# Optimization experiments

Hardware: AMD Instinct MI355X
Metric: run time of the kernel (lower is better)

Reference implementation:

```python
import jax, jax.numpy as jnp
import numpy as np

D_MODEL = 1024
N_HEADS = 16
HEAD_DIM = D_MODEL // N_HEADS
ROPE_BASE = 10000.0


def setup_inputs() -> dict:
    key = jax.random.key(0)
    k1, k2, k3 = jax.random.split(key, 3)
    B, T = 4, 2048
    s = 0.02
    x = jax.random.normal(k1, (B, T, D_MODEL), dtype=jnp.float32)
    w_qkv = jax.random.normal(k2, (D_MODEL, 3 * D_MODEL), dtype=jnp.float32) * s
    b_qkv = jnp.zeros((3 * D_MODEL,), dtype=jnp.float32)
    w_out = jax.random.normal(k3, (D_MODEL, D_MODEL), dtype=jnp.float32) * s
    b_out = jnp.zeros((D_MODEL,), dtype=jnp.float32)
    return {"x": x, "w_qkv": w_qkv, "b_qkv": b_qkv, "w_out": w_out, "b_out": b_out}


def _rope(q, k):
    # q, k: [B, H, T, D]; standard rotate-half RoPE, base 10000
    T, D = q.shape[-2], q.shape[-1]
    inv_freq = 1.0 / (ROPE_BASE ** (jnp.arange(0, D, 2, dtype=jnp.float32) / D))
    freqs = jnp.arange(T, dtype=jnp.float32)[:, None] * inv_freq[None, :]  # [T, D/2]
    emb = jnp.concatenate([freqs, freqs], axis=-1)                         # [T, D]
    cos, sin = jnp.cos(emb), jnp.sin(emb)

    def rot_half(x):
        x1, x2 = x[..., : D // 2], x[..., D // 2 :]
        return jnp.concatenate([-x2, x1], axis=-1)

    q = q * cos + rot_half(q) * sin
    k = k * cos + rot_half(k) * sin
    return q, k


def reference(x, w_qkv, b_qkv, w_out, b_out):
    B, T, C = x.shape
    H, D = N_HEADS, HEAD_DIM
    qkv = x @ w_qkv + b_qkv                      # [B, T, 3C]
    q, k, v = jnp.split(qkv, 3, axis=-1)
    # [B, T, C] -> [B, H, T, D]
    q = q.reshape(B, T, H, D).transpose(0, 2, 1, 3)
    k = k.reshape(B, T, H, D).transpose(0, 2, 1, 3)
    v = v.reshape(B, T, H, D).transpose(0, 2, 1, 3)
    q, k = _rope(q, k)
    scores = jnp.einsum("bhqd,bhkd->bhqk", q, k) / jnp.sqrt(jnp.asarray(D, x.dtype))
    causal = jnp.tril(jnp.ones((T, T), dtype=bool))
    scores = jnp.where(causal, scores, jnp.asarray(-1e30, scores.dtype))
    attn = jax.nn.softmax(scores, axis=-1)
    out = jnp.einsum("bhqk,bhkd->bhqd", attn, v)  # [B, H, T, D]
    out = out.transpose(0, 2, 1, 3).reshape(B, T, C)
    return out @ w_out + b_out
```

## Files before the change

kernel.cpp:

```cpp
#include <hip/hip_runtime.h>
#include <stdint.h>

#define B_SZ 4
#define T_SZ 2048
#define H_SZ 16
#define D_SZ 64
#define C_SZ 1024
#define N3_SZ 3072
#define M_SZ (B_SZ * T_SZ)

using bf16x8 = __attribute__((ext_vector_type(8))) __bf16;
using f32x4  = __attribute__((ext_vector_type(4))) float;
using f32x16 = __attribute__((ext_vector_type(16))) float;
using uivec2 = __attribute__((ext_vector_type(2))) unsigned int;
using uivec4 = __attribute__((ext_vector_type(4))) unsigned int;

__device__ __forceinline__ unsigned short f2bf(float f) {
    union { float f; unsigned int u; } v; v.f = f;
    unsigned int r = v.u + 0x7FFFu + ((v.u >> 16) & 1u);
    return (unsigned short)(r >> 16);
}
__device__ __forceinline__ unsigned int pack_bf2(float lo, float hi) {
    return (unsigned int)f2bf(lo) | ((unsigned int)f2bf(hi) << 16);
}

__device__ __forceinline__ void async16(const void* g, void* l) {
    __builtin_amdgcn_global_load_lds((const __attribute__((address_space(1))) void*)g,
                                     (__attribute__((address_space(3))) void*)l, 16, 0, 0);
}
__device__ __forceinline__ f32x4 mfma16(bf16x8 a, bf16x8 b, f32x4 c) {
    return __builtin_amdgcn_mfma_f32_16x16x32_bf16(a, b, c, 0, 0, 0);
}
__device__ __forceinline__ f32x16 mfma32(bf16x8 a, bf16x8 b, f32x16 c) {
    return __builtin_amdgcn_mfma_f32_32x32x16_bf16(a, b, c, 0, 0, 0);
}
__device__ __forceinline__ f32x16 zero16() {
    f32x16 z;
#pragma unroll
    for (int i = 0; i < 16; i++) z[i] = 0.f;
    return z;
}

__global__ void k_f32_to_bf16(const float4* __restrict__ in, uint2* __restrict__ out, int n4) {
    int i = blockIdx.x * blockDim.x + threadIdx.x;
    int stride = gridDim.x * blockDim.x;
    for (; i < n4; i += stride) {
        float4 v = in[i];
        uint2 o;
        o.x = pack_bf2(v.x, v.y);
        o.y = pack_bf2(v.z, v.w);
        out[i] = o;
    }
}

__global__ void k_transpose_bf16(const float* __restrict__ in, unsigned short* __restrict__ out,
                                 int K, int N) {
    __shared__ float tile[32][33];
    int n0 = blockIdx.x * 32, k0 = blockIdx.y * 32;
    int tx = threadIdx.x & 31, ty = threadIdx.x >> 5;
#pragma unroll
    for (int j = 0; j < 32; j += 8)
        tile[ty + j][tx] = in[(size_t)(k0 + ty + j) * N + (n0 + tx)];
    __syncthreads();
#pragma unroll
    for (int j = 0; j < 32; j += 8)
        out[(size_t)(n0 + ty + j) * K + (k0 + tx)] = f2bf(tile[tx][ty + j]);
}

__global__ void k_transpose_v(const unsigned short* __restrict__ qkv,
                              unsigned short* __restrict__ vt) {
    __shared__ unsigned short tile[32][36];
    int t0 = blockIdx.x * 32, d0 = blockIdx.y * 32, bh = blockIdx.z;
    int b = bh >> 4, h = bh & 15;
    int row = threadIdx.x >> 3, ch = threadIdx.x & 7;
    const unsigned short* src =
        qkv + (size_t)(b * T_SZ + t0 + row) * N3_SZ + 2 * C_SZ + h * D_SZ + d0 + ch * 4;
    *(uint2*)&tile[row][ch * 4] = *(const uint2*)src;
    __syncthreads();
    unsigned short o[4];
#pragma unroll
    for (int i = 0; i < 4; i++) o[i] = tile[ch * 4 + i][row];
    *(uint2*)(vt + ((size_t)bh * 64 + d0 + row) * T_SZ + t0 + ch * 4) = *(uint2*)o;
}

__global__ void k_rope_table(float* __restrict__ rtab) {
    int i = blockIdx.x * blockDim.x + threadIdx.x;
    if (i >= T_SZ * 32) return;
    int t = i >> 5, fq = i & 31;
    float invf = powf(10000.0f, -(float)fq / 32.0f);
    float ang = (float)t * invf;
    rtab[t * 64 + fq * 2]     = cosf(ang);
    rtab[t * 64 + fq * 2 + 1] = sinf(ang);
}

#define GEMM_PHASE_TAIL()                                    \
    __builtin_amdgcn_s_barrier();                            \
    asm volatile("s_waitcnt lgkmcnt(0)" ::: "memory");       \
    __builtin_amdgcn_sched_barrier(0);                       \
    __builtin_amdgcn_s_setprio(1);

#define GEMM_PHASE_END()                                     \
    __builtin_amdgcn_s_setprio(0);                           \
    __builtin_amdgcn_s_barrier();

#define MFMA8(MF, A0, A1)                                    \
    acc[MF][0] = mfma16(A0, b00, acc[MF][0]);                \
    acc[MF][1] = mfma16(A0, b10, acc[MF][1]);                \
    acc[MF][2] = mfma16(A0, b20, acc[MF][2]);                \
    acc[MF][3] = mfma16(A0, b30, acc[MF][3]);                \
    acc[MF][0] = mfma16(A1, b01, acc[MF][0]);                \
    acc[MF][1] = mfma16(A1, b11, acc[MF][1]);                \
    acc[MF][2] = mfma16(A1, b21, acc[MF][2]);                \
    acc[MF][3] = mfma16(A1, b31, acc[MF][3]);

#define GEMM_BODY(Kdim)                                                                    \
    const int tid = threadIdx.x;                                                           \
    const int wave = tid >> 6, lane = tid & 63;                                            \
    const int lcol = lane & 15, lrow = lane >> 4;                                          \
    const int wm = wave >> 2, wn = wave & 3;                                               \
    const int sx = lcol & 7;                                                               \
    const int srow = tid >> 3;                                                             \
    const int sch = (tid & 7) ^ (srow & 7);                                                \
    const unsigned short* Asrc = A + (size_t)(m0 + srow) * (Kdim) + sch * 8;               \
    const unsigned short* Bsrc = BT + (size_t)(n0 + srow) * (Kdim) + sch * 8;              \
    const int ldst = tid * 8;                                                              \
    f32x4 acc[4][4];                                                                       \
    _Pragma("unroll") for (int i = 0; i < 4; i++)                                          \
        _Pragma("unroll") for (int j = 0; j < 4; j++) acc[i][j] = (f32x4){0.f,0.f,0.f,0.f};\
    SU_B(0,0,0); SU_B(0,1,0); SU_B(0,2,0); SU_B(0,3,0); SU_A(0,0,0); SU_A(0,1,0);          \
    SU_B(1,0,64); SU_B(1,1,64); SU_B(1,2,64); SU_B(1,3,64); SU_A(1,0,64); SU_A(1,1,64);    \
    asm volatile("s_waitcnt vmcnt(6)" ::: "memory");                                       \
    __builtin_amdgcn_s_barrier();                                                          \
    const int NT = (Kdim) >> 6;                                                            \
    for (int t = 0; t < NT; ++t) {                                                         \
        const int cur = t % 3;                                                             \
        int nx2 = cur + 2; if (nx2 >= 3) nx2 -= 3;                                         \
        const unsigned short* Acur = As + cur * 8192;                                      \
        const unsigned short* Bcur = Bs + cur * 16384;                                     \
        const size_t kn = (size_t)(t + 2) * 64;                                            \
        const bool more2 = (t + 2 < NT);                                                   \
        bf16x8 b00, b01, b10, b11, b20, b21, b30, b31;                                     \
        {                                                                                  \
            bf16x8 a0 = LD_A(0, 0), a1 = LD_A(0, 1);                                       \
            b00 = LD_B(0, 0); b01 = LD_B(0, 1);                                            \
            b10 = LD_B(1, 0); b11 = LD_B(1, 1);                                            \
            b20 = LD_B(2, 0); b21 = LD_B(2, 1);                                            \
            b30 = LD_B(3, 0); b31 = LD_B(3, 1);                                            \
            if (more2) { SU_B(nx2, 0, kn); SU_B(nx2, 1, kn); }                             \
            GEMM_PHASE_TAIL(); MFMA8(0, a0, a1); GEMM_PHASE_END();                         \
        }                                                                                  \
        {                                                                                  \
            bf16x8 a0 = LD_A(1, 0), a1 = LD_A(1, 1);                                       \
            if (more2) { SU_B(nx2, 2, kn); SU_B(nx2, 3, kn); }                             \
            GEMM_PHASE_TAIL(); MFMA8(1, a0, a1); GEMM_PHASE_END();                         \
        }                                                                                  \
        {                                                                                  \
            bf16x8 a0 = LD_A(2, 0), a1 = LD_A(2, 1);                                       \
            if (more2) { SU_A(nx2, 0, kn); }                                               \
            GEMM_PHASE_TAIL(); MFMA8(2, a0, a1); GEMM_PHASE_END();                         \
        }                                                                                  \
        {                                                                                  \
            bf16x8 a0 = LD_A(3, 0), a1 = LD_A(3, 1);                                       \
            if (more2) { SU_A(nx2, 1, kn); }                                               \
            if (more2) asm volatile("s_waitcnt vmcnt(6)" ::: "memory");                    \
            else       asm volatile("s_waitcnt vmcnt(0)" ::: "memory");                    \
            GEMM_PHASE_TAIL(); MFMA8(3, a0, a1); GEMM_PHASE_END();                         \
        }                                                                                  \
    }

#define SU_A(BI, Q, KO) async16(Asrc + (size_t)(Q) * 64 * KD + (KO), \
                                As + (BI) * 8192 + (Q) * 4096 + ldst)
#define SU_B(BI, Q, KO) async16(Bsrc + (size_t)(Q) * 64 * KD + (KO), \
                                Bs + (BI) * 16384 + (Q) * 4096 + ldst)
#define LD_A(MF, KS) (*reinterpret_cast<const bf16x8*>( \
    Acur + ((wm * 64 + (MF) * 16 + lcol)) * 64 + ((((KS) * 4 + lrow) ^ sx) * 8)))
#define LD_B(NF, KS) (*reinterpret_cast<const bf16x8*>( \
    Bcur + ((wn * 64 + (NF) * 16 + lcol)) * 64 + ((((KS) * 4 + lrow) ^ sx) * 8)))

__global__ __launch_bounds__(512, 2) void k_gemmqkv(const unsigned short* __restrict__ A,
                                                    const unsigned short* __restrict__ BT,
                                                    const float* __restrict__ bias,
                                                    unsigned short* __restrict__ qkv,
                                                    const float* __restrict__ rtab) {
    extern __shared__ unsigned short lds[];
    unsigned short* As = lds;
    unsigned short* Bs = lds + 3 * 8192;
#define KD C_SZ
    int orig = blockIdx.x + gridDim.x * blockIdx.y;
    int lin = (orig & 7) * 96 + (orig >> 3);
    const int n0 = (lin % 12) * 256, m0 = (lin / 12) * 128;
    GEMM_BODY(C_SZ)
#undef KD

    const int cb = n0 + wn * 64;
    float bv[4];
#pragma unroll
    for (int nf = 0; nf < 4; nf++) bv[nf] = bias[cb + nf * 16 + lcol];
    if (cb < 2 * C_SZ) {
        const float scl = (cb < C_SZ) ? 0.125f * 1.4426950408889634f : 1.0f;
#pragma unroll
        for (int mf = 0; mf < 4; mf++) {
#pragma unroll
            for (int r = 0; r < 4; r++) {
                int row = m0 + wm * 64 + mf * 16 + lrow * 4 + r;
                int t = row & (T_SZ - 1);
#pragma unroll
                for (int p = 0; p < 2; p++) {
                    int fq = p * 16 + lcol;
                    float2 cs = *(const float2*)(rtab + t * 64 + fq * 2);
                    float a  = acc[mf][p][r]     + bv[p];
                    float bb = acc[mf][p + 2][r] + bv[p + 2];
                    float lo = (a * cs.x - bb * cs.y) * scl;
                    float hi = (bb * cs.x + a * cs.y) * scl;
                    qkv[(size_t)row * N3_SZ + cb + fq]      = f2bf(lo);
                    qkv[(size_t)row * N3_SZ + cb + fq + 32] = f2bf(hi);
                }
            }
        }
    } else {
#pragma unroll
        for (int nf = 0; nf < 4; nf++) {
#pragma unroll
            for (int mf = 0; mf < 4; mf++) {
#pragma unroll
                for (int r = 0; r < 4; r++) {
                    int row = m0 + wm * 64 + mf * 16 + lrow * 4 + r;
                    qkv[(size_t)row * N3_SZ + cb + nf * 16 + lcol] =
                        f2bf(acc[mf][nf][r] + bv[nf]);
                }
            }
        }
    }
}

__global__ __launch_bounds__(512, 2) void k_gemmout(const unsigned short* __restrict__ A,
                                                    const unsigned short* __restrict__ BT,
                                                    const float* __restrict__ bias,
                                                    float* __restrict__ Cout) {
    extern __shared__ unsigned short lds[];
    unsigned short* As = lds;
    unsigned short* Bs = lds + 3 * 8192;
#define KD C_SZ
    int orig = blockIdx.x + gridDim.x * blockIdx.y;
    int lin = (orig & 7) * 32 + (orig >> 3);
    const int n0 = (lin % 4) * 256, m0 = (lin / 4) * 128;
    GEMM_BODY(C_SZ)
#undef KD
    const int cb = n0 + wn * 64;
#pragma unroll
    for (int nf = 0; nf < 4; nf++) {
        int col = cb + nf * 16 + lcol;
        float bv = bias[col];
#pragma unroll
        for (int mf = 0; mf < 4; mf++) {
#pragma unroll
            for (int r = 0; r < 4; r++) {
                int row = m0 + wm * 64 + mf * 16 + lrow * 4 + r;
                Cout[(size_t)row * C_SZ + col] = acc[mf][nf][r] + bv;
            }
        }
    }
}

#undef SU_A
#undef SU_B
#undef LD_A
#undef LD_B

__global__ __launch_bounds__(512, 4) void k_attn(const unsigned short* __restrict__ qkv,
                                                 const unsigned short* __restrict__ vt,
                                                 unsigned short* __restrict__ attn_out) {
    __shared__ __align__(16) unsigned short lds[16384];
    int orig = blockIdx.x + gridDim.x * blockIdx.y;
    int lin = (orig & 7) * 64 + (orig >> 3);
    const int pr = lin & 7, bh = lin >> 3;
    const int b = bh >> 4, h = bh & 15;
    const int qtA = pr, qtB = 15 - pr;
    const int tid = threadIdx.x;
    const int w = tid >> 6, lane = tid & 63;
    const int l31 = lane & 31, hi = lane >> 5;
    const int sx = l31 & 7;
    const int wsel = w >> 2;
    const int wq0 = (wsel ? qtB : qtA) * 128 + (w & 3) * 32;
    const int qg = wq0 + l31;

    const size_t gbase = (size_t)b * T_SZ * N3_SZ;
    const size_t vbase = (size_t)bh * 64 * T_SZ;

#pragma unroll
    for (int L = 0; L < 4; L++) {
        int flat = L * 512 + tid;
        int row = flat >> 3, ch = flat & 7;
        int qrow = (row < 128) ? (qtA * 128 + row) : (qtB * 128 + row - 128);
        int chs = ch ^ (row & 7);
        async16(qkv + gbase + (size_t)qrow * N3_SZ + h * D_SZ + chs * 8, lds + flat * 8);
    }
    asm volatile("s_waitcnt vmcnt(0)" ::: "memory");
    __builtin_amdgcn_s_barrier();
    bf16x8 qf[4];
#pragma unroll
    for (int s = 0; s < 4; s++)
        qf[s] = *reinterpret_cast<const bf16x8*>(
            lds + wsel * 8192 + ((w & 3) * 32 + l31) * 64 + ((2 * s + hi) ^ sx) * 8);
    asm volatile("s_waitcnt lgkmcnt(0)" ::: "memory");
    __builtin_amdgcn_sched_barrier(0);
    __builtin_amdgcn_s_barrier();

    const int srow = tid >> 3;
    const int schs = (tid & 7) ^ (srow & 7);
    const unsigned short* ksrc0 = qkv + gbase + (size_t)srow * N3_SZ + C_SZ + h * D_SZ + schs * 8;
    const unsigned short* vsrc0 = vt + vbase + (size_t)srow * T_SZ + schs * 8;
#define STAGE(KV0, BI)                                                      \
    do {                                                                    \
        async16(ksrc0 + (size_t)(KV0) * N3_SZ, lds + (BI) * 8192 + tid * 8);\
        async16(vsrc0 + (KV0), lds + (BI) * 8192 + 4096 + tid * 8);         \
    } while (0)

    f32x16 accO[2];
    accO[0] = zero16();
    accO[1] = zero16();
    float lsum = 0.f;

    STAGE(0, 0);
    const int nkv = 32 - 2 * pr;
    for (int kv = 0; kv < nkv; kv++) {
        const int cur = kv & 1;
        const int kv0 = kv * 64;
        if (kv + 1 < nkv) {
            STAGE(kv0 + 64, cur ^ 1);
            asm volatile("s_waitcnt vmcnt(2)" ::: "memory");
        } else {
            asm volatile("s_waitcnt vmcnt(0)" ::: "memory");
        }
        __builtin_amdgcn_s_barrier();
        asm volatile("" ::: "memory");

        if (kv0 <= wq0 + 31) {
            const unsigned short* Kb = lds + cur * 8192;
            const unsigned short* Vb = lds + cur * 8192 + 4096;
            const bool diag = (kv0 + 63) > wq0;
            __builtin_amdgcn_s_setprio(1);
#pragma unroll
            for (int kk = 0; kk < 2; kk++) {
                f32x16 sc = zero16();
                const unsigned short* krow = Kb + (kk * 32 + l31) * 64;
#pragma unroll
                for (int s = 0; s < 4; s++) {
                    bf16x8 kf = *reinterpret_cast<const bf16x8*>(krow + ((2 * s + hi) ^ sx) * 8);
                    sc = mfma32(kf, qf[s], sc);
                }
                const int kvkk = kv0 + kk * 32 + 4 * hi;
                unsigned int wd[4][2];
#pragma unroll
                for (int i = 0; i < 16; i += 2) {
                    float p0 = __builtin_amdgcn_exp2f(sc[i]);
                    float p1 = __builtin_amdgcn_exp2f(sc[i + 1]);
                    if (diag) {
                        int kg = kvkk + (i & 3) + 8 * (i >> 2);
                        p0 = (kg > qg) ? 0.f : p0;
                        p1 = (kg + 1 > qg) ? 0.f : p1;
                    }
                    lsum += p0 + p1;
                    unsigned int wv;
                    asm("v_cvt_pk_bf16_f32 %0, %1, %2" : "=v"(wv) : "v"(p0), "v"(p1));
                    wd[i >> 2][(i >> 1) & 1] = wv;
                }
#pragma unroll
                for (int s = 0; s < 2; s++) {
                    uivec2 r0 = __builtin_amdgcn_permlane32_swap(wd[2 * s][0], wd[2 * s + 1][0],
                                                                 false, false);
                    uivec2 r1 = __builtin_amdgcn_permlane32_swap(wd[2 * s][1], wd[2 * s + 1][1],
                                                                 false, false);
                    uivec4 frv = {r0.x, r1.x, r0.y, r1.y};
                    bf16x8 pfrag = __builtin_bit_cast(bf16x8, frv);
                    const int ks = kk * 2 + s;
#pragma unroll
                    for (int dt = 0; dt < 2; dt++) {
                        bf16x8 vf = *reinterpret_cast<const bf16x8*>(
                            Vb + (dt * 32 + l31) * 64 + ((2 * ks + hi) ^ sx) * 8);
                        accO[dt] = mfma32(vf, pfrag, accO[dt]);
                    }
                }
            }
            __builtin_amdgcn_s_setprio(0);
        }
        asm volatile("" ::: "memory");
        __builtin_amdgcn_s_barrier();
    }
#undef STAGE

    __syncthreads();
    float lt = lsum + __shfl_xor(lsum, 32, 64);
    float linv = 1.0f / lt;
    unsigned int* ow = (unsigned int*)lds + w * 1024;
#pragma unroll
    for (int dt = 0; dt < 2; dt++) {
#pragma unroll
        for (int i = 0; i < 16; i += 2) {
            float v0 = accO[dt][i] * linv;
            float v1 = accO[dt][i + 1] * linv;
            unsigned int wv;
            asm("v_cvt_pk_bf16_f32 %0, %1, %2" : "=v"(wv) : "v"(v0), "v"(v1));
            int idx = ((i & 3) + 8 * (i >> 2) + 4 * hi + 32 * dt) >> 1;
            ow[l31 * 32 + (idx ^ (sx << 2))] = wv;
        }
    }
    int q2 = lane >> 1;
    int c0 = (lane & 1) * 4;
    unsigned short* orow = attn_out + (size_t)(b * T_SZ + wq0 + q2) * C_SZ + h * D_SZ;
#pragma unroll
    for (int j = 0; j < 4; j++) {
        int c = c0 + j;
        uint4 val = *(const uint4*)(ow + q2 * 32 + ((c ^ (q2 & 7)) * 4));
        *(uint4*)(orow + c * 8) = val;
    }
}

extern "C" void kernel_launch(void* const* d_in, const int* in_sizes, int n_in,
                              void* d_out, int out_size, void* d_ws, size_t ws_size,
                              hipStream_t stream) {
    (void)in_sizes; (void)n_in; (void)out_size;
    const float* x     = (const float*)d_in[0];
    const float* w_qkv = (const float*)d_in[1];
    const float* b_qkv = (const float*)d_in[2];
    const float* w_out = (const float*)d_in[3];
    const float* b_out = (const float*)d_in[4];
    float* out = (float*)d_out;

    unsigned short* xb    = (unsigned short*)d_ws;
    unsigned short* wqkvT = xb + (size_t)M_SZ * C_SZ;
    unsigned short* woutT = wqkvT + (size_t)N3_SZ * C_SZ;
    unsigned short* qkv   = woutT + (size_t)C_SZ * C_SZ;
    unsigned short* attn  = qkv + (size_t)M_SZ * N3_SZ;
    float* rtab = (float*)(attn + (size_t)M_SZ * C_SZ);
    unsigned short* vtb = xb;
    size_t needed = (size_t)((char*)(rtab + T_SZ * 64) - (char*)d_ws);
    if (ws_size < needed) return;

    hipFuncSetAttribute((const void*)k_gemmqkv,
                        hipFuncAttributeMaxDynamicSharedMemorySize, 147456);
    hipFuncSetAttribute((const void*)k_gemmout,
                        hipFuncAttributeMaxDynamicSharedMemorySize, 147456);

    k_f32_to_bf16<<<2048, 256, 0, stream>>>((const float4*)x, (uint2*)xb, M_SZ * C_SZ / 4);
    k_transpose_bf16<<<dim3(N3_SZ / 32, C_SZ / 32), 256, 0, stream>>>(w_qkv, wqkvT, C_SZ, N3_SZ);
    k_transpose_bf16<<<dim3(C_SZ / 32, C_SZ / 32), 256, 0, stream>>>(w_out, woutT, C_SZ, C_SZ);
    k_rope_table<<<(T_SZ * 32 + 255) / 256, 256, 0, stream>>>(rtab);
    k_gemmqkv<<<dim3(12, 64), 512, 147456, stream>>>(xb, wqkvT, b_qkv, qkv, rtab);
    k_transpose_v<<<dim3(T_SZ / 32, 2, B_SZ * H_SZ), 256, 0, stream>>>(qkv, vtb);
    k_attn<<<dim3(8, 64), 512, 0, stream>>>(qkv, vtb, attn);
    k_gemmout<<<dim3(4, 64), 512, 147456, stream>>>(attn, woutT, b_out, out);
}
```

Baseline: 176.9 us.

## Fuse V transpose into QKV GEMM epilogue and split late attention tiles across warp groups

The QKV GEMM epilogue now writes Q and K into separate compact buffers and writes V directly in transposed per-head layout, which removes the standalone V transpose kernel and its extra pass over memory. The attention kernel is restructured so that once the early query tile is finished, both warp groups share the remaining KV blocks of the late tile, each taking half of every block. Their partial outputs and row sums are then combined through LDS. This is meant to balance work between the two warp groups under the causal mask. It costs extra registers for a second accumulator set plus several extra barriers and an LDS reduction.

```diff
diff --git a/kernel.cpp b/kernel.cpp
--- a/kernel.cpp
+++ b/kernel.cpp
@@ -65,22 +65,6 @@
 #pragma unroll
     for (int j = 0; j < 32; j += 8)
         out[(size_t)(n0 + ty + j) * K + (k0 + tx)] = f2bf(tile[tx][ty + j]);
-}
-
-__global__ void k_transpose_v(const unsigned short* __restrict__ qkv,
-                              unsigned short* __restrict__ vt) {
-    __shared__ unsigned short tile[32][36];
-    int t0 = blockIdx.x * 32, d0 = blockIdx.y * 32, bh = blockIdx.z;
-    int b = bh >> 4, h = bh & 15;
-    int row = threadIdx.x >> 3, ch = threadIdx.x & 7;
-    const unsigned short* src =
-        qkv + (size_t)(b * T_SZ + t0 + row) * N3_SZ + 2 * C_SZ + h * D_SZ + d0 + ch * 4;
-    *(uint2*)&tile[row][ch * 4] = *(const uint2*)src;
-    __syncthreads();
-    unsigned short o[4];
-#pragma unroll
-    for (int i = 0; i < 4; i++) o[i] = tile[ch * 4 + i][row];
-    *(uint2*)(vt + ((size_t)bh * 64 + d0 + row) * T_SZ + t0 + ch * 4) = *(uint2*)o;
 }
 
 __global__ void k_rope_table(float* __restrict__ rtab) {
@@ -180,7 +164,9 @@
 __global__ __launch_bounds__(512, 2) void k_gemmqkv(const unsigned short* __restrict__ A,
                                                     const unsigned short* __restrict__ BT,
                                                     const float* __restrict__ bias,
-                                                    unsigned short* __restrict__ qkv,
+                                                    unsigned short* __restrict__ qp,
+                                                    unsigned short* __restrict__ kp,
+                                                    unsigned short* __restrict__ vtp,
                                                     const float* __restrict__ rtab) {
     extern __shared__ unsigned short lds[];
     unsigned short* As = lds;
@@ -198,6 +184,8 @@
     for (int nf = 0; nf < 4; nf++) bv[nf] = bias[cb + nf * 16 + lcol];
     if (cb < 2 * C_SZ) {
         const float scl = (cb < C_SZ) ? 0.125f * 1.4426950408889634f : 1.0f;
+        unsigned short* dst = (cb < C_SZ) ? qp : kp;
+        const int cbl = cb & (C_SZ - 1);
 #pragma unroll
         for (int mf = 0; mf < 4; mf++) {
 #pragma unroll
@@ -212,22 +200,27 @@
                     float bb = acc[mf][p + 2][r] + bv[p + 2];
                     float lo = (a * cs.x - bb * cs.y) * scl;
                     float hi = (bb * cs.x + a * cs.y) * scl;
-                    qkv[(size_t)row * N3_SZ + cb + fq]      = f2bf(lo);
-                    qkv[(size_t)row * N3_SZ + cb + fq + 32] = f2bf(hi);
+                    dst[(size_t)row * C_SZ + cbl + fq]      = f2bf(lo);
+                    dst[(size_t)row * C_SZ + cbl + fq + 32] = f2bf(hi);
                 }
             }
         }
     } else {
+        const int hh = (cb - 2 * C_SZ) >> 6;
+        const int bb = m0 >> 11;
+        const int bhv = bb * H_SZ + hh;
+        const int t0w = (m0 & (T_SZ - 1)) + wm * 64;
 #pragma unroll
         for (int nf = 0; nf < 4; nf++) {
+            const int d = nf * 16 + lcol;
+            unsigned short* vrow = vtp + ((size_t)bhv * 64 + d) * T_SZ + t0w;
 #pragma unroll
             for (int mf = 0; mf < 4; mf++) {
-#pragma unroll
-                for (int r = 0; r < 4; r++) {
-                    int row = m0 + wm * 64 + mf * 16 + lrow * 4 + r;
-                    qkv[(size_t)row * N3_SZ + cb + nf * 16 + lcol] =
-                        f2bf(acc[mf][nf][r] + bv[nf]);
-                }
+                int t = mf * 16 + lrow * 4;
+                uint2 o;
+                o.x = pack_bf2(acc[mf][nf][0] + bv[nf], acc[mf][nf][1] + bv[nf]);
+                o.y = pack_bf2(acc[mf][nf][2] + bv[nf], acc[mf][nf][3] + bv[nf]);
+                *(uint2*)(vrow + t) = o;
             }
         }
     }
@@ -267,8 +260,9 @@
 #undef LD_A
 #undef LD_B
 
-__global__ __launch_bounds__(512, 4) void k_attn(const unsigned short* __restrict__ qkv,
-                                                 const unsigned short* __restrict__ vt,
+__global__ __launch_bounds__(512, 4) void k_attn(const unsigned short* __restrict__ qp,
+                                                 const unsigned short* __restrict__ kp,
+                                                 const unsigned short* __restrict__ vtp,
                                                  unsigned short* __restrict__ attn_out) {
     __shared__ __align__(16) unsigned short lds[16384];
     int orig = blockIdx.x + gridDim.x * blockIdx.y;
@@ -280,12 +274,10 @@
     const int w = tid >> 6, lane = tid & 63;
     const int l31 = lane & 31, hi = lane >> 5;
     const int sx = l31 & 7;
-    const int wsel = w >> 2;
-    const int wq0 = (wsel ? qtB : qtA) * 128 + (w & 3) * 32;
-    const int qg = wq0 + l31;
-
-    const size_t gbase = (size_t)b * T_SZ * N3_SZ;
-    const size_t vbase = (size_t)bh * 64 * T_SZ;
+    const int wsel = w >> 2, wsub = w & 3;
+    const int wq0A = qtA * 128 + wsub * 32;
+    const int wq0B = qtB * 128 + wsub * 32;
+    const int wq0E = wsel ? wq0B : wq0A;
 
 #pragma unroll
     for (int L = 0; L < 4; L++) {
@@ -293,36 +285,85 @@
         int row = flat >> 3, ch = flat & 7;
         int qrow = (row < 128) ? (qtA * 128 + row) : (qtB * 128 + row - 128);
         int chs = ch ^ (row & 7);
-        async16(qkv + gbase + (size_t)qrow * N3_SZ + h * D_SZ + chs * 8, lds + flat * 8);
+        async16(qp + ((size_t)(b * T_SZ + qrow)) * C_SZ + h * D_SZ + chs * 8, lds + flat * 8);
     }
     asm volatile("s_waitcnt vmcnt(0)" ::: "memory");
     __builtin_amdgcn_s_barrier();
-    bf16x8 qf[4];
-#pragma unroll
-    for (int s = 0; s < 4; s++)
-        qf[s] = *reinterpret_cast<const bf16x8*>(
-            lds + wsel * 8192 + ((w & 3) * 32 + l31) * 64 + ((2 * s + hi) ^ sx) * 8);
+    bf16x8 qfE[4], qfB[4];
+#pragma unroll
+    for (int s = 0; s < 4; s++) {
+        qfE[s] = *reinterpret_cast<const bf16x8*>(
+            lds + wsel * 8192 + (wsub * 32 + l31) * 64 + ((2 * s + hi) ^ sx) * 8);
+        qfB[s] = *reinterpret_cast<const bf16x8*>(
+            lds + 8192 + (wsub * 32 + l31) * 64 + ((2 * s + hi) ^ sx) * 8);
+    }
     asm volatile("s_waitcnt lgkmcnt(0)" ::: "memory");
     __builtin_amdgcn_sched_barrier(0);
     __builtin_amdgcn_s_barrier();
 
     const int srow = tid >> 3;
     const int schs = (tid & 7) ^ (srow & 7);
-    const unsigned short* ksrc0 = qkv + gbase + (size_t)srow * N3_SZ + C_SZ + h * D_SZ + schs * 8;
-    const unsigned short* vsrc0 = vt + vbase + (size_t)srow * T_SZ + schs * 8;
-#define STAGE(KV0, BI)                                                      \
-    do {                                                                    \
-        async16(ksrc0 + (size_t)(KV0) * N3_SZ, lds + (BI) * 8192 + tid * 8);\
-        async16(vsrc0 + (KV0), lds + (BI) * 8192 + 4096 + tid * 8);         \
+    const unsigned short* ksrc0 = kp + ((size_t)b * T_SZ + srow) * C_SZ + h * D_SZ + schs * 8;
+    const unsigned short* vsrc0 = vtp + (size_t)bh * 64 * T_SZ + (size_t)srow * T_SZ + schs * 8;
+#define STAGE(KV0, BI)                                                        \
+    do {                                                                      \
+        async16(ksrc0 + (size_t)(KV0) * C_SZ, lds + (BI) * 8192 + tid * 8);   \
+        async16(vsrc0 + (KV0), lds + (BI) * 8192 + 4096 + tid * 8);           \
     } while (0)
 
-    f32x16 accO[2];
-    accO[0] = zero16();
-    accO[1] = zero16();
-    float lsum = 0.f;
+#define KKBODY(KK, QF, ACC, LSUM, WQ0)                                                     \
+    do {                                                                                   \
+        f32x16 sc = zero16();                                                              \
+        const unsigned short* krow = Kb + ((KK) * 32 + l31) * 64;                          \
+        _Pragma("unroll")                                                                  \
+        for (int s = 0; s < 4; s++) {                                                      \
+            bf16x8 kf = *reinterpret_cast<const bf16x8*>(krow + ((2 * s + hi) ^ sx) * 8);  \
+            sc = mfma32(kf, QF[s], sc);                                                    \
+        }                                                                                  \
+        const bool diag = (kv0 + (KK) * 32 + 31) > (WQ0);                                  \
+        const int kvkk = kv0 + (KK) * 32 + 4 * hi;                                         \
+        const int qg = (WQ0) + l31;                                                        \
+        unsigned int wd[4][2];                                                             \
+        _Pragma("unroll")                                                                  \
+        for (int i = 0; i < 16; i += 2) {                                                  \
+            float p0 = __builtin_amdgcn_exp2f(sc[i]);                                      \
+            float p1 = __builtin_amdgcn_exp2f(sc[i + 1]);                                  \
+            if (diag) {                                                                    \
+                int kg = kvkk + (i & 3) + 8 * (i >> 2);                                    \
+                p0 = (kg > qg) ? 0.f : p0;                                                 \
+                p1 = (kg + 1 > qg) ? 0.f : p1;                                             \
+            }                                                                              \
+            LSUM += p0 + p1;                                                               \
+            unsigned int wv;                                                               \
+            asm("v_cvt_pk_bf16_f32 %0, %1, %2" : "=v"(wv) : "v"(p0), "v"(p1));             \
+            wd[i >> 2][(i >> 1) & 1] = wv;                                                 \
+        }                                                                                  \
+        _Pragma("unroll")                                                                  \
+        for (int s = 0; s < 2; s++) {                                                      \
+            uivec2 r0 = __builtin_amdgcn_permlane32_swap(wd[2 * s][0], wd[2 * s + 1][0],   \
+                                                         false, false);                    \
+            uivec2 r1 = __builtin_amdgcn_permlane32_swap(wd[2 * s][1], wd[2 * s + 1][1],   \
+                                                         false, false);                    \
+            uivec4 frv = {r0.x, r1.x, r0.y, r1.y};                                         \
+            bf16x8 pfrag = __builtin_bit_cast(bf16x8, frv);                                \
+            const int ks = (KK) * 2 + s;                                                   \
+            _Pragma("unroll")                                                              \
+            for (int dt = 0; dt < 2; dt++) {                                               \
+                bf16x8 vf = *reinterpret_cast<const bf16x8*>(                              \
+                    Vb + (dt * 32 + l31) * 64 + ((2 * ks + hi) ^ sx) * 8);                 \
+                ACC[dt] = mfma32(vf, pfrag, ACC[dt]);                                      \
+            }                                                                              \
+        }                                                                                  \
+    } while (0)
+
+    f32x16 accE[2], accL[2];
+    accE[0] = zero16(); accE[1] = zero16();
+    accL[0] = zero16(); accL[1] = zero16();
+    float lsumE = 0.f, lsumL = 0.f;
 
     STAGE(0, 0);
-    const int nkv = 32 - 2 * pr;
+    const int thrA = 2 * pr + 2;
+    const int nkv = 2 * qtB + 2;
     for (int kv = 0; kv < nkv; kv++) {
         const int cur = kv & 1;
         const int kv0 = kv * 64;
@@ -335,70 +376,69 @@
         __builtin_amdgcn_s_barrier();
         asm volatile("" ::: "memory");
 
-        if (kv0 <= wq0 + 31) {
-            const unsigned short* Kb = lds + cur * 8192;
-            const unsigned short* Vb = lds + cur * 8192 + 4096;
-            const bool diag = (kv0 + 63) > wq0;
-            __builtin_amdgcn_s_setprio(1);
-#pragma unroll
-            for (int kk = 0; kk < 2; kk++) {
-                f32x16 sc = zero16();
-                const unsigned short* krow = Kb + (kk * 32 + l31) * 64;
-#pragma unroll
-                for (int s = 0; s < 4; s++) {
-                    bf16x8 kf = *reinterpret_cast<const bf16x8*>(krow + ((2 * s + hi) ^ sx) * 8);
-                    sc = mfma32(kf, qf[s], sc);
-                }
-                const int kvkk = kv0 + kk * 32 + 4 * hi;
-                unsigned int wd[4][2];
-#pragma unroll
-                for (int i = 0; i < 16; i += 2) {
-                    float p0 = __builtin_amdgcn_exp2f(sc[i]);
-                    float p1 = __builtin_amdgcn_exp2f(sc[i + 1]);
-                    if (diag) {
-                        int kg = kvkk + (i & 3) + 8 * (i >> 2);
-                        p0 = (kg > qg) ? 0.f : p0;
-                        p1 = (kg + 1 > qg) ? 0.f : p1;
-                    }
-                    lsum += p0 + p1;
-                    unsigned int wv;
-                    asm("v_cvt_pk_bf16_f32 %0, %1, %2" : "=v"(wv) : "v"(p0), "v"(p1));
-                    wd[i >> 2][(i >> 1) & 1] = wv;
-                }
-#pragma unroll
-                for (int s = 0; s < 2; s++) {
-                    uivec2 r0 = __builtin_amdgcn_permlane32_swap(wd[2 * s][0], wd[2 * s + 1][0],
-                                                                 false, false);
-                    uivec2 r1 = __builtin_amdgcn_permlane32_swap(wd[2 * s][1], wd[2 * s + 1][1],
-                                                                 false, false);
-                    uivec4 frv = {r0.x, r1.x, r0.y, r1.y};
-                    bf16x8 pfrag = __builtin_bit_cast(bf16x8, frv);
-                    const int ks = kk * 2 + s;
-#pragma unroll
-                    for (int dt = 0; dt < 2; dt++) {
-                        bf16x8 vf = *reinterpret_cast<const bf16x8*>(
-                            Vb + (dt * 32 + l31) * 64 + ((2 * ks + hi) ^ sx) * 8);
-                        accO[dt] = mfma32(vf, pfrag, accO[dt]);
-                    }
-                }
-            }
-            __builtin_amdgcn_s_setprio(0);
+        const unsigned short* Kb = lds + cur * 8192;
+        const unsigned short* Vb = lds + cur * 8192 + 4096;
+        if (kv < thrA) {
+            if (kv0 <= wq0E + 31) {
+                __builtin_amdgcn_s_setprio(1);
+                KKBODY(0, qfE, accE, lsumE, wq0E);
+                KKBODY(1, qfE, accE, lsumE, wq0E);
+                __builtin_amdgcn_s_setprio(0);
+            }
+        } else {
+            if (kv0 + wsel * 32 <= wq0B + 31) {
+                __builtin_amdgcn_s_setprio(1);
+                KKBODY(wsel, qfB, accL, lsumL, wq0B);
+                __builtin_amdgcn_s_setprio(0);
+            }
         }
         asm volatile("" ::: "memory");
         __builtin_amdgcn_s_barrier();
     }
 #undef STAGE
-
-    __syncthreads();
-    float lt = lsum + __shfl_xor(lsum, 32, 64);
+#undef KKBODY
+
+    __syncthreads();
+    if (!wsel) {
+        float4* dstp = (float4*)lds + (size_t)w * 512;
+#pragma unroll
+        for (int dt = 0; dt < 2; dt++)
+#pragma unroll
+            for (int i = 0; i < 4; i++) {
+                float4 q = {accL[dt][4 * i], accL[dt][4 * i + 1],
+                            accL[dt][4 * i + 2], accL[dt][4 * i + 3]};
+                dstp[(dt * 4 + i) * 64 + lane] = q;
+            }
+    }
+    __syncthreads();
+    if (wsel) {
+        const float4* srcp = (const float4*)lds + (size_t)(w - 4) * 512;
+#pragma unroll
+        for (int dt = 0; dt < 2; dt++)
+#pragma unroll
+            for (int i = 0; i < 4; i++) {
+                float4 q = srcp[(dt * 4 + i) * 64 + lane];
+                accE[dt][4 * i]     += accL[dt][4 * i]     + q.x;
+                accE[dt][4 * i + 1] += accL[dt][4 * i + 1] + q.y;
+                accE[dt][4 * i + 2] += accL[dt][4 * i + 2] + q.z;
+                accE[dt][4 * i + 3] += accL[dt][4 * i + 3] + q.w;
+            }
+    }
+    __syncthreads();
+    if (!wsel) ((float*)lds)[w * 64 + lane] = lsumL;
+    __syncthreads();
+    float lsumF = lsumE + (wsel ? (lsumL + ((float*)lds)[(w - 4) * 64 + lane]) : 0.f);
+    __syncthreads();
+
+    float lt = lsumF + __shfl_xor(lsumF, 32, 64);
     float linv = 1.0f / lt;
     unsigned int* ow = (unsigned int*)lds + w * 1024;
 #pragma unroll
     for (int dt = 0; dt < 2; dt++) {
 #pragma unroll
         for (int i = 0; i < 16; i += 2) {
-            float v0 = accO[dt][i] * linv;
-            float v1 = accO[dt][i + 1] * linv;
+            float v0 = accE[dt][i] * linv;
+            float v1 = accE[dt][i + 1] * linv;
             unsigned int wv;
             asm("v_cvt_pk_bf16_f32 %0, %1, %2" : "=v"(wv) : "v"(v0), "v"(v1));
             int idx = ((i & 3) + 8 * (i >> 2) + 4 * hi + 32 * dt) >> 1;
@@ -407,7 +447,7 @@
     }
     int q2 = lane >> 1;
     int c0 = (lane & 1) * 4;
-    unsigned short* orow = attn_out + (size_t)(b * T_SZ + wq0 + q2) * C_SZ + h * D_SZ;
+    unsigned short* orow = attn_out + (size_t)(b * T_SZ + wq0E + q2) * C_SZ + h * D_SZ;
 #pragma unroll
     for (int j = 0; j < 4; j++) {
         int c = c0 + j;
@@ -430,10 +470,11 @@
     unsigned short* xb    = (unsigned short*)d_ws;
     unsigned short* wqkvT = xb + (size_t)M_SZ * C_SZ;
     unsigned short* woutT = wqkvT + (size_t)N3_SZ * C_SZ;
-    unsigned short* qkv   = woutT + (size_t)C_SZ * C_SZ;
-    unsigned short* attn  = qkv + (size_t)M_SZ * N3_SZ;
+    unsigned short* qp    = woutT + (size_t)C_SZ * C_SZ;
+    unsigned short* kpp   = qp + (size_t)M_SZ * C_SZ;
+    unsigned short* vtp   = kpp + (size_t)M_SZ * C_SZ;
+    unsigned short* attn  = vtp + (size_t)M_SZ * C_SZ;
     float* rtab = (float*)(attn + (size_t)M_SZ * C_SZ);
-    unsigned short* vtb = xb;
     size_t needed = (size_t)((char*)(rtab + T_SZ * 64) - (char*)d_ws);
     if (ws_size < needed) return;
 
@@ -446,8 +487,7 @@
     k_transpose_bf16<<<dim3(N3_SZ / 32, C_SZ / 32), 256, 0, stream>>>(w_qkv, wqkvT, C_SZ, N3_SZ);
     k_transpose_bf16<<<dim3(C_SZ / 32, C_SZ / 32), 256, 0, stream>>>(w_out, woutT, C_SZ, C_SZ);
     k_rope_table<<<(T_SZ * 32 + 255) / 256, 256, 0, stream>>>(rtab);
-    k_gemmqkv<<<dim3(12, 64), 512, 147456, stream>>>(xb, wqkvT, b_qkv, qkv, rtab);
-    k_transpose_v<<<dim3(T_SZ / 32, 2, B_SZ * H_SZ), 256, 0, stream>>>(qkv, vtb);
-    k_attn<<<dim3(8, 64), 512, 0, stream>>>(qkv, vtb, attn);
+    k_gemmqkv<<<dim3(12, 64), 512, 147456, stream>>>(xb, wqkvT, b_qkv, qp, kpp, vtp, rtab);
+    k_attn<<<dim3(8, 64), 512, 0, stream>>>(qp, kpp, vtp, attn);
     k_gemmout<<<dim3(4, 64), 512, 147456, stream>>>(attn, woutT, b_out, out);
 }
```

Result: slower. 241.4 us (+36.5%).

## Fuse V transpose into QKV GEMM epilogue and split Q/K/V buffers

Applied to the files above, without the earlier changes.

The QKV GEMM epilogue now writes V directly in transposed [B,H,D,T] layout with packed 8-byte stores, which removes the separate V-transpose kernel and its extra read and write of V. Q and K go to separate [M,C] buffers instead of one interleaved [M,3C] buffer, so attention loads use a smaller row stride. The V stores in the epilogue become strided across rows of length T, and the workspace grows because V no longer reuses the xb buffer.

```diff
diff --git a/kernel.cpp b/kernel.cpp
--- a/kernel.cpp
+++ b/kernel.cpp
@@ -65,22 +65,6 @@
 #pragma unroll
     for (int j = 0; j < 32; j += 8)
         out[(size_t)(n0 + ty + j) * K + (k0 + tx)] = f2bf(tile[tx][ty + j]);
-}
-
-__global__ void k_transpose_v(const unsigned short* __restrict__ qkv,
-                              unsigned short* __restrict__ vt) {
-    __shared__ unsigned short tile[32][36];
-    int t0 = blockIdx.x * 32, d0 = blockIdx.y * 32, bh = blockIdx.z;
-    int b = bh >> 4, h = bh & 15;
-    int row = threadIdx.x >> 3, ch = threadIdx.x & 7;
-    const unsigned short* src =
-        qkv + (size_t)(b * T_SZ + t0 + row) * N3_SZ + 2 * C_SZ + h * D_SZ + d0 + ch * 4;
-    *(uint2*)&tile[row][ch * 4] = *(const uint2*)src;
-    __syncthreads();
-    unsigned short o[4];
-#pragma unroll
-    for (int i = 0; i < 4; i++) o[i] = tile[ch * 4 + i][row];
-    *(uint2*)(vt + ((size_t)bh * 64 + d0 + row) * T_SZ + t0 + ch * 4) = *(uint2*)o;
 }
 
 __global__ void k_rope_table(float* __restrict__ rtab) {
@@ -180,7 +164,9 @@
 __global__ __launch_bounds__(512, 2) void k_gemmqkv(const unsigned short* __restrict__ A,
                                                     const unsigned short* __restrict__ BT,
                                                     const float* __restrict__ bias,
-                                                    unsigned short* __restrict__ qkv,
+                                                    unsigned short* __restrict__ qp,
+                                                    unsigned short* __restrict__ kp,
+                                                    unsigned short* __restrict__ vtp,
                                                     const float* __restrict__ rtab) {
     extern __shared__ unsigned short lds[];
     unsigned short* As = lds;
@@ -198,6 +184,8 @@
     for (int nf = 0; nf < 4; nf++) bv[nf] = bias[cb + nf * 16 + lcol];
     if (cb < 2 * C_SZ) {
         const float scl = (cb < C_SZ) ? 0.125f * 1.4426950408889634f : 1.0f;
+        unsigned short* dst = (cb < C_SZ) ? qp : kp;
+        const int cbl = cb & (C_SZ - 1);
 #pragma unroll
         for (int mf = 0; mf < 4; mf++) {
 #pragma unroll
@@ -212,22 +200,27 @@
                     float bb = acc[mf][p + 2][r] + bv[p + 2];
                     float lo = (a * cs.x - bb * cs.y) * scl;
                     float hi = (bb * cs.x + a * cs.y) * scl;
-                    qkv[(size_t)row * N3_SZ + cb + fq]      = f2bf(lo);
-                    qkv[(size_t)row * N3_SZ + cb + fq + 32] = f2bf(hi);
+                    dst[(size_t)row * C_SZ + cbl + fq]      = f2bf(lo);
+                    dst[(size_t)row * C_SZ + cbl + fq + 32] = f2bf(hi);
                 }
             }
         }
     } else {
+        const int hh = (cb - 2 * C_SZ) >> 6;
+        const int bb = m0 >> 11;
+        const int bhv = bb * H_SZ + hh;
+        const int t0w = (m0 & (T_SZ - 1)) + wm * 64;
 #pragma unroll
         for (int nf = 0; nf < 4; nf++) {
+            const int d = nf * 16 + lcol;
+            unsigned short* vrow = vtp + ((size_t)bhv * 64 + d) * T_SZ + t0w;
 #pragma unroll
             for (int mf = 0; mf < 4; mf++) {
-#pragma unroll
-                for (int r = 0; r < 4; r++) {
-                    int row = m0 + wm * 64 + mf * 16 + lrow * 4 + r;
-                    qkv[(size_t)row * N3_SZ + cb + nf * 16 + lcol] =
-                        f2bf(acc[mf][nf][r] + bv[nf]);
-                }
+                int t = mf * 16 + lrow * 4;
+                uint2 o;
+                o.x = pack_bf2(acc[mf][nf][0] + bv[nf], acc[mf][nf][1] + bv[nf]);
+                o.y = pack_bf2(acc[mf][nf][2] + bv[nf], acc[mf][nf][3] + bv[nf]);
+                *(uint2*)(vrow + t) = o;
             }
         }
     }
@@ -267,8 +260,9 @@
 #undef LD_A
 #undef LD_B
 
-__global__ __launch_bounds__(512, 4) void k_attn(const unsigned short* __restrict__ qkv,
-                                                 const unsigned short* __restrict__ vt,
+__global__ __launch_bounds__(512, 4) void k_attn(const unsigned short* __restrict__ qp,
+                                                 const unsigned short* __restrict__ kp,
+                                                 const unsigned short* __restrict__ vtp,
                                                  unsigned short* __restrict__ attn_out) {
     __shared__ __align__(16) unsigned short lds[16384];
     int orig = blockIdx.x + gridDim.x * blockIdx.y;
@@ -284,16 +278,13 @@
     const int wq0 = (wsel ? qtB : qtA) * 128 + (w & 3) * 32;
     const int qg = wq0 + l31;
 
-    const size_t gbase = (size_t)b * T_SZ * N3_SZ;
-    const size_t vbase = (size_t)bh * 64 * T_SZ;
-
 #pragma unroll
     for (int L = 0; L < 4; L++) {
         int flat = L * 512 + tid;
         int row = flat >> 3, ch = flat & 7;
         int qrow = (row < 128) ? (qtA * 128 + row) : (qtB * 128 + row - 128);
         int chs = ch ^ (row & 7);
-        async16(qkv + gbase + (size_t)qrow * N3_SZ + h * D_SZ + chs * 8, lds + flat * 8);
+        async16(qp + ((size_t)(b * T_SZ + qrow)) * C_SZ + h * D_SZ + chs * 8, lds + flat * 8);
     }
     asm volatile("s_waitcnt vmcnt(0)" ::: "memory");
     __builtin_amdgcn_s_barrier();
@@ -308,12 +299,12 @@
 
     const int srow = tid >> 3;
     const int schs = (tid & 7) ^ (srow & 7);
-    const unsigned short* ksrc0 = qkv + gbase + (size_t)srow * N3_SZ + C_SZ + h * D_SZ + schs * 8;
-    const unsigned short* vsrc0 = vt + vbase + (size_t)srow * T_SZ + schs * 8;
-#define STAGE(KV0, BI)                                                      \
-    do {                                                                    \
-        async16(ksrc0 + (size_t)(KV0) * N3_SZ, lds + (BI) * 8192 + tid * 8);\
-        async16(vsrc0 + (KV0), lds + (BI) * 8192 + 4096 + tid * 8);         \
+    const unsigned short* ksrc0 = kp + ((size_t)b * T_SZ + srow) * C_SZ + h * D_SZ + schs * 8;
+    const unsigned short* vsrc0 = vtp + (size_t)bh * 64 * T_SZ + (size_t)srow * T_SZ + schs * 8;
+#define STAGE(KV0, BI)                                                        \
+    do {                                                                      \
+        async16(ksrc0 + (size_t)(KV0) * C_SZ, lds + (BI) * 8192 + tid * 8);   \
+        async16(vsrc0 + (KV0), lds + (BI) * 8192 + 4096 + tid * 8);           \
     } while (0)
 
     f32x16 accO[2];
@@ -430,10 +421,11 @@
     unsigned short* xb    = (unsigned short*)d_ws;
     unsigned short* wqkvT = xb + (size_t)M_SZ * C_SZ;
     unsigned short* woutT = wqkvT + (size_t)N3_SZ * C_SZ;
-    unsigned short* qkv   = woutT + (size_t)C_SZ * C_SZ;
-    unsigned short* attn  = qkv + (size_t)M_SZ * N3_SZ;
+    unsigned short* qp    = woutT + (size_t)C_SZ * C_SZ;
+    unsigned short* kpp   = qp + (size_t)M_SZ * C_SZ;
+    unsigned short* vtp   = kpp + (size_t)M_SZ * C_SZ;
+    unsigned short* attn  = vtp + (size_t)M_SZ * C_SZ;
     float* rtab = (float*)(attn + (size_t)M_SZ * C_SZ);
-    unsigned short* vtb = xb;
     size_t needed = (size_t)((char*)(rtab + T_SZ * 64) - (char*)d_ws);
     if (ws_size < needed) return;
 
@@ -446,8 +438,7 @@
     k_transpose_bf16<<<dim3(N3_SZ / 32, C_SZ / 32), 256, 0, stream>>>(w_qkv, wqkvT, C_SZ, N3_SZ);
     k_transpose_bf16<<<dim3(C_SZ / 32, C_SZ / 32), 256, 0, stream>>>(w_out, woutT, C_SZ, C_SZ);
     k_rope_table<<<(T_SZ * 32 + 255) / 256, 256, 0, stream>>>(rtab);
-    k_gemmqkv<<<dim3(12, 64), 512, 147456, stream>>>(xb, wqkvT, b_qkv, qkv, rtab);
-    k_transpose_v<<<dim3(T_SZ / 32, 2, B_SZ * H_SZ), 256, 0, stream>>>(qkv, vtb);
-    k_attn<<<dim3(8, 64), 512, 0, stream>>>(qkv, vtb, attn);
+    k_gemmqkv<<<dim3(12, 64), 512, 147456, stream>>>(xb, wqkvT, b_qkv, qp, kpp, vtp, rtab);
+    k_attn<<<dim3(8, 64), 512, 0, stream>>>(qp, kpp, vtp, attn);
     k_gemmout<<<dim3(4, 64), 512, 147456, stream>>>(attn, woutT, b_out, out);
 }
```

Result: faster. 172.9 us (-2.3%).
